# Optimization experiments

Hardware: AMD Instinct MI355X
Metric: run time of the kernel (lower is better)

Reference implementation:

```python
import jax, jax.numpy as jnp
import numpy as np

T, D_IN, NE = 131072, 1024, 64

def setup_inputs() -> dict:
    key = jax.random.key(0)
    k1, k2 = jax.random.split(key)
    x = jax.random.normal(k1, (T, D_IN), dtype=jnp.float32)
    W = jax.random.normal(k2, (NE, D_IN), dtype=jnp.float32) * (1.0 / np.sqrt(D_IN))
    return {"x": x, "W": W, "top_k": 2}

def reference(x, W, top_k):
    # fp32 router logits: [T, Ne]
    logits = jnp.einsum('td,ed->te', x.astype(jnp.float32), W.astype(jnp.float32))
    k = min(int(top_k), W.shape[0])
    vals, idx = jax.lax.top_k(logits, k)           # [T, k] each
    w = jax.nn.softmax(vals, axis=-1).astype(x.dtype)
    return (idx, w)
```

## Files before the change

### kernel.cpp

```cpp
#include <hip/hip_runtime.h>
#include <math.h>

constexpr int T_TOKENS = 131072;
constexpr int D        = 1024;
constexpr float EPS_GAP = 1e-3f;

typedef __attribute__((ext_vector_type(8))) short bf16x8;
typedef __attribute__((ext_vector_type(4))) float f32x4;
typedef __bf16 bf16v8 __attribute__((ext_vector_type(8)));
typedef float  f32v8  __attribute__((ext_vector_type(8)));

__device__ __forceinline__ void split2(const float4 lo, const float4 hi,
                                       bf16x8& p0, bf16x8& p1) {
    f32v8 f = {lo.x, lo.y, lo.z, lo.w, hi.x, hi.y, hi.z, hi.w};
    bf16v8 h0 = __builtin_convertvector(f, bf16v8);
    f32v8 back = __builtin_convertvector(h0, f32v8);
    bf16v8 h1 = __builtin_convertvector(f - back, bf16v8);
    p0 = __builtin_bit_cast(bf16x8, h0);
    p1 = __builtin_bit_cast(bf16x8, h1);
}

__global__ void prep_w(const float* __restrict__ W, bf16x8* __restrict__ wpl) {
    const int g = blockIdx.x;
    const int c = threadIdx.x >> 6;
    const int l = threadIdx.x & 63;
    const int e  = c * 16 + (l & 15);
    const int k0 = g * 32 + (l >> 4) * 8;
    const float4 lo = *(const float4*)(W + (long)e * D + k0);
    const float4 hi = *(const float4*)(W + (long)e * D + k0 + 4);
    bf16x8 p0, p1; split2(lo, hi, p0, p1);
    const int base = ((g * 4 + c) * 2) * 64 + l;
    wpl[base]      = p0;
    wpl[base + 64] = p1;
}

__global__ __launch_bounds__(256, 2)
void router_mfma(const float* __restrict__ x, const bf16x8* __restrict__ wpl,
                 float* __restrict__ out, unsigned* __restrict__ wcnt,
                 unsigned* __restrict__ wlist, unsigned cap)
{
    __shared__ __align__(16) char Xs[4][2][8192];

    const int tid = threadIdx.x;
    const int wv  = tid >> 6;
    const int l   = tid & 63;
    const int lg  = l >> 4;
    const int lr  = l & 15;
    const long t0 = (long)blockIdx.x * 128 + wv * 32;
    const int swz = (lr & 7) << 4;

    f32x4 acc[2][4];
#pragma unroll
    for (int a = 0; a < 2; ++a)
#pragma unroll
        for (int c = 0; c < 4; ++c) acc[a][c] = f32x4{0.f, 0.f, 0.f, 0.f};

    const int sil = (l & 15) * 16;
    const int sir = l >> 4;
    const char* xb = (const char*)x;

#define STAGE(S, BUF)                                                          \
    {                                                                          \
        _Pragma("unroll")                                                      \
        for (int i = 0; i < 8; ++i) {                                          \
            const int rr = 4 * i + sir;                                        \
            const char* src = xb + (t0 + rr) * 4096L + (S) * 256               \
                              + (sil ^ ((rr & 7) << 4));                       \
            char* dst = &Xs[wv][BUF][i * 1024];                                \
            __builtin_amdgcn_global_load_lds(                                  \
                (const __attribute__((address_space(1))) void*)src,            \
                (__attribute__((address_space(3))) void*)dst, 16, 0, 0);       \
        }                                                                      \
    }

#define SUBSTEP(SUB, W)                                                        \
    {                                                                          \
        const int c0 = (SUB) * 128 + lg * 32;                                  \
        const float4 lo0 = *(const float4*)(wb + lr * 256 + ((c0) ^ swz));     \
        const float4 hi0 = *(const float4*)(wb + lr * 256 + ((c0 + 16) ^ swz));\
        const float4 lo1 = *(const float4*)(wb + (16 + lr) * 256 + ((c0) ^ swz));     \
        const float4 hi1 = *(const float4*)(wb + (16 + lr) * 256 + ((c0 + 16) ^ swz));\
        bf16x8 a00, a01, a10, a11;                                             \
        split2(lo0, hi0, a00, a01);                                            \
        split2(lo1, hi1, a10, a11);                                            \
        _Pragma("unroll")                                                      \
        for (int c = 0; c < 4; ++c) {                                          \
            acc[0][c] = __builtin_amdgcn_mfma_f32_16x16x32_bf16(a00, W[c*2+0], acc[0][c], 0, 0, 0); \
            acc[0][c] = __builtin_amdgcn_mfma_f32_16x16x32_bf16(a01, W[c*2+0], acc[0][c], 0, 0, 0); \
            acc[0][c] = __builtin_amdgcn_mfma_f32_16x16x32_bf16(a00, W[c*2+1], acc[0][c], 0, 0, 0); \
            acc[1][c] = __builtin_amdgcn_mfma_f32_16x16x32_bf16(a10, W[c*2+0], acc[1][c], 0, 0, 0); \
            acc[1][c] = __builtin_amdgcn_mfma_f32_16x16x32_bf16(a11, W[c*2+0], acc[1][c], 0, 0, 0); \
            acc[1][c] = __builtin_amdgcn_mfma_f32_16x16x32_bf16(a10, W[c*2+1], acc[1][c], 0, 0, 0); \
        }                                                                      \
    }

    STAGE(0, 0);

#pragma unroll 1
    for (int s = 0; s < 16; ++s) {
        const int buf = s & 1;
        bf16x8 w0[8], w1[8];
#pragma unroll
        for (int c = 0; c < 4; ++c) {
            w0[c * 2 + 0] = wpl[(size_t)(2 * s) * 512 + (c * 2 + 0) * 64 + l];
            w0[c * 2 + 1] = wpl[(size_t)(2 * s) * 512 + (c * 2 + 1) * 64 + l];
            w1[c * 2 + 0] = wpl[(size_t)(2 * s + 1) * 512 + (c * 2 + 0) * 64 + l];
            w1[c * 2 + 1] = wpl[(size_t)(2 * s + 1) * 512 + (c * 2 + 1) * 64 + l];
        }
        const int sn = (s + 1 < 16) ? s + 1 : 15;
        if (buf) { STAGE(sn, 0) } else { STAGE(sn, 1) }
        asm volatile("s_waitcnt vmcnt(24)" ::: "memory");
        __builtin_amdgcn_sched_barrier(0);
        const char* wb = &Xs[wv][buf][0];
        SUBSTEP(0, w0)
        SUBSTEP(1, w1)
    }
#undef SUBSTEP
#undef STAGE

#pragma unroll
    for (int a = 0; a < 2; ++a)
#pragma unroll
    for (int r = 0; r < 4; ++r) {
        float v1 = acc[a][0][r]; int i1 = lr;
        float v2 = -INFINITY;    int i2 = 1 << 20;
        float v3 = -INFINITY;
#pragma unroll
        for (int c = 1; c < 4; ++c) {
            const float v = acc[a][c][r]; const int e = lr + 16 * c;
            if (v > v1)      { v3 = v2; v2 = v1; i2 = i1; v1 = v; i1 = e; }
            else if (v > v2) { v3 = v2; v2 = v;  i2 = e; }
            else if (v > v3) { v3 = v; }
        }
#pragma unroll
        for (int m = 8; m >= 1; m >>= 1) {
            const float ov1 = __shfl_xor(v1, m);
            const int   oi1 = __shfl_xor(i1, m);
            const float ov2 = __shfl_xor(v2, m);
            const int   oi2 = __shfl_xor(i2, m);
            const float ov3 = __shfl_xor(v3, m);
            const bool tv = v1 >= ov1;
            const float x2 = tv ? v2 : ov2, x3 = tv ? v3 : ov3;
            const float y1 = tv ? ov1 : v1, y2 = tv ? ov2 : v2;
            const float nv3 = (x2 >= y1) ? fmaxf(x3, y1) : fmaxf(x2, y2);
            const bool aw = (ov1 > v1) || (ov1 == v1 && oi1 < i1);
            const float nv1 = aw ? ov1 : v1; const int ni1 = aw ? oi1 : i1;
            const float c1v = aw ? v1  : ov1; const int c1i = aw ? i1  : oi1;
            const float c2v = aw ? ov2 : v2;  const int c2i = aw ? oi2 : i2;
            const bool bw = (c1v > c2v) || (c1v == c2v && c1i < c2i);
            v1 = nv1; i1 = ni1;
            v2 = bw ? c1v : c2v; i2 = bw ? c1i : c2i;
            v3 = nv3;
        }
        if (lr == 0) {
            const long t = t0 + a * 16 + lg * 4 + r;
            const float e  = expf(v2 - v1);
            const float dn = 1.0f + e;
            out[t * 2 + 0] = (float)i1;
            out[t * 2 + 1] = (float)i2;
            out[(long)T_TOKENS * 2 + t * 2 + 0] = 1.0f / dn;
            out[(long)T_TOKENS * 2 + t * 2 + 1] = e / dn;
            if (v1 - v2 < EPS_GAP || v2 - v3 < EPS_GAP) {
                const unsigned p = atomicAdd(wcnt, 1u);
                if (p < cap) wlist[p] = (unsigned)t;
            }
        }
    }
}

__global__ __launch_bounds__(256)
void router_fixup(const float* __restrict__ x, const float* __restrict__ W,
                  float* __restrict__ out, const unsigned* __restrict__ wcnt,
                  const unsigned* __restrict__ wlist, unsigned cap)
{
    __shared__ float ps[4][64];
    unsigned cnt = wcnt[0]; if (cnt > cap) cnt = cap;
    const int wv = threadIdx.x >> 6;
    const int l  = threadIdx.x & 63;
    const int kb = (wv == 0) ? 0 : (wv == 1) ? 320 : (wv == 2) ? 640 : 832;
    const int ke = (wv == 0) ? 320 : (wv == 1) ? 640 : (wv == 2) ? 832 : 1024;

    for (unsigned it = blockIdx.x; it < cnt; it += gridDim.x) {
        const long t = (long)wlist[it];
        const float* xr = x + t * (long)D;
        const float* wr = W + (long)l * D;
        float accP = 0.f;
#pragma unroll 4
        for (int k = kb; k < ke; k += 4) {
            const float4 xv = *(const float4*)(xr + k);
            const float4 wvv = *(const float4*)(wr + k);
            accP = fmaf(xv.x, wvv.x, accP);
            accP = fmaf(xv.y, wvv.y, accP);
            accP = fmaf(xv.z, wvv.z, accP);
            accP = fmaf(xv.w, wvv.w, accP);
        }
        ps[wv][l] = accP;
        __syncthreads();
        if (wv == 0) {
            const float accT = __fadd_rn(__fadd_rn(__fadd_rn(ps[0][l], ps[1][l]), ps[2][l]), ps[3][l]);
            float v1 = accT; int i1 = l;
            float v2 = -INFINITY; int i2 = 1 << 20;
#pragma unroll
            for (int m = 32; m >= 1; m >>= 1) {
                const float ov1 = __shfl_xor(v1, m);
                const int   oi1 = __shfl_xor(i1, m);
                const float ov2 = __shfl_xor(v2, m);
                const int   oi2 = __shfl_xor(i2, m);
                const bool aw = (ov1 > v1) || (ov1 == v1 && oi1 < i1);
                const float nv1 = aw ? ov1 : v1; const int ni1 = aw ? oi1 : i1;
                const float c1v = aw ? v1  : ov1; const int c1i = aw ? i1  : oi1;
                const float c2v = aw ? ov2 : v2;  const int c2i = aw ? oi2 : i2;
                const bool bw = (c1v > c2v) || (c1v == c2v && c1i < c2i);
                v1 = nv1; i1 = ni1;
                v2 = bw ? c1v : c2v; i2 = bw ? c1i : c2i;
            }
            if (l == 0) {
                const float e  = expf(v2 - v1);
                const float dn = 1.0f + e;
                out[t * 2 + 0] = (float)i1;
                out[t * 2 + 1] = (float)i2;
                out[(long)T_TOKENS * 2 + t * 2 + 0] = 1.0f / dn;
                out[(long)T_TOKENS * 2 + t * 2 + 1] = e / dn;
            }
        }
        __syncthreads();
    }
}

extern "C" void kernel_launch(void* const* d_in, const int* in_sizes, int n_in,
                              void* d_out, int out_size, void* d_ws, size_t ws_size,
                              hipStream_t stream) {
    const float* x = (const float*)d_in[0];
    const float* W = (const float*)d_in[1];
    float* out = (float*)d_out;

    unsigned* wcnt  = (unsigned*)d_ws;
    bf16x8*   wpl   = (bf16x8*)((char*)d_ws + 1024);
    unsigned* wlist = (unsigned*)((char*)d_ws + 1024 + 262144);
    size_t rem = (ws_size - 1024 - 262144) / 4;
    unsigned cap = (unsigned)(rem > (1u << 22) ? (1u << 22) : rem);

    (void)hipMemsetAsync(d_ws, 0, 64, stream);
    prep_w<<<dim3(32), dim3(256), 0, stream>>>(W, wpl);
    router_mfma<<<dim3(T_TOKENS / 128), dim3(256), 0, stream>>>(x, wpl, out, wcnt, wlist, cap);
    router_fixup<<<dim3(512), dim3(256), 0, stream>>>(x, W, out, wcnt, wlist, cap);
}
```

Baseline: 191.4 us.

## Halve tokens per wave and double K-chunk per pipeline stage

Each wave now handles 16 tokens instead of 32, and each stage loads 128 floats of K per token instead of 64, giving 8 pipeline iterations with 4 substeps each. The grid doubles to T/64 blocks, so there is more parallelism and fewer, larger stages with less loop overhead. The cost is that the W fragments fetched per iteration are reused across only one 16-token tile instead of two, doubling W traffic per token, and 32 bf16x8 W registers are held at once, which adds register pressure.

Result: slower. 203.9 us (+6.5%).

```diff
diff --git a/kernel.cpp b/kernel.cpp
--- a/kernel.cpp
+++ b/kernel.cpp
@@ -46,25 +46,21 @@
     const int l   = tid & 63;
     const int lg  = l >> 4;
     const int lr  = l & 15;
-    const long t0 = (long)blockIdx.x * 128 + wv * 32;
+    const long t0 = (long)blockIdx.x * 64 + wv * 16;
     const int swz = (lr & 7) << 4;
-
-    f32x4 acc[2][4];
-#pragma unroll
-    for (int a = 0; a < 2; ++a)
-#pragma unroll
-        for (int c = 0; c < 4; ++c) acc[a][c] = f32x4{0.f, 0.f, 0.f, 0.f};
-
-    const int sil = (l & 15) * 16;
-    const int sir = l >> 4;
+    const int sil = (l & 31) * 16;
     const char* xb = (const char*)x;
+
+    f32x4 acc[4];
+#pragma unroll
+    for (int c = 0; c < 4; ++c) acc[c] = f32x4{0.f, 0.f, 0.f, 0.f};
 
 #define STAGE(S, BUF)                                                          \
     {                                                                          \
         _Pragma("unroll")                                                      \
         for (int i = 0; i < 8; ++i) {                                          \
-            const int rr = 4 * i + sir;                                        \
-            const char* src = xb + (t0 + rr) * 4096L + (S) * 256               \
+            const int rr = 2 * i + (l >> 5);                                   \
+            const char* src = xb + (t0 + rr) * 4096L + (S) * 512               \
                               + (sil ^ ((rr & 7) << 4));                       \
             char* dst = &Xs[wv][BUF][i * 1024];                                \
             __builtin_amdgcn_global_load_lds(                                  \
@@ -73,61 +69,52 @@
         }                                                                      \
     }
 
-#define SUBSTEP(SUB, W)                                                        \
+#define SUBSTEP(SUB)                                                           \
     {                                                                          \
         const int c0 = (SUB) * 128 + lg * 32;                                  \
-        const float4 lo0 = *(const float4*)(wb + lr * 256 + ((c0) ^ swz));     \
-        const float4 hi0 = *(const float4*)(wb + lr * 256 + ((c0 + 16) ^ swz));\
-        const float4 lo1 = *(const float4*)(wb + (16 + lr) * 256 + ((c0) ^ swz));     \
-        const float4 hi1 = *(const float4*)(wb + (16 + lr) * 256 + ((c0 + 16) ^ swz));\
-        bf16x8 a00, a01, a10, a11;                                             \
-        split2(lo0, hi0, a00, a01);                                            \
-        split2(lo1, hi1, a10, a11);                                            \
+        const float4 lo = *(const float4*)(wb + lr * 512 + (c0 ^ swz));        \
+        const float4 hi = *(const float4*)(wb + lr * 512 + ((c0 + 16) ^ swz)); \
+        bf16x8 a0, a1;                                                         \
+        split2(lo, hi, a0, a1);                                                \
         _Pragma("unroll")                                                      \
         for (int c = 0; c < 4; ++c) {                                          \
-            acc[0][c] = __builtin_amdgcn_mfma_f32_16x16x32_bf16(a00, W[c*2+0], acc[0][c], 0, 0, 0); \
-            acc[0][c] = __builtin_amdgcn_mfma_f32_16x16x32_bf16(a01, W[c*2+0], acc[0][c], 0, 0, 0); \
-            acc[0][c] = __builtin_amdgcn_mfma_f32_16x16x32_bf16(a00, W[c*2+1], acc[0][c], 0, 0, 0); \
-            acc[1][c] = __builtin_amdgcn_mfma_f32_16x16x32_bf16(a10, W[c*2+0], acc[1][c], 0, 0, 0); \
-            acc[1][c] = __builtin_amdgcn_mfma_f32_16x16x32_bf16(a11, W[c*2+0], acc[1][c], 0, 0, 0); \
-            acc[1][c] = __builtin_amdgcn_mfma_f32_16x16x32_bf16(a10, W[c*2+1], acc[1][c], 0, 0, 0); \
+            acc[c] = __builtin_amdgcn_mfma_f32_16x16x32_bf16(a0, w[SUB][c*2+0], acc[c], 0, 0, 0); \
+            acc[c] = __builtin_amdgcn_mfma_f32_16x16x32_bf16(a1, w[SUB][c*2+0], acc[c], 0, 0, 0); \
+            acc[c] = __builtin_amdgcn_mfma_f32_16x16x32_bf16(a0, w[SUB][c*2+1], acc[c], 0, 0, 0); \
         }                                                                      \
     }
 
     STAGE(0, 0);
 
 #pragma unroll 1
-    for (int s = 0; s < 16; ++s) {
+    for (int s = 0; s < 8; ++s) {
         const int buf = s & 1;
-        bf16x8 w0[8], w1[8];
-#pragma unroll
-        for (int c = 0; c < 4; ++c) {
-            w0[c * 2 + 0] = wpl[(size_t)(2 * s) * 512 + (c * 2 + 0) * 64 + l];
-            w0[c * 2 + 1] = wpl[(size_t)(2 * s) * 512 + (c * 2 + 1) * 64 + l];
-            w1[c * 2 + 0] = wpl[(size_t)(2 * s + 1) * 512 + (c * 2 + 0) * 64 + l];
-            w1[c * 2 + 1] = wpl[(size_t)(2 * s + 1) * 512 + (c * 2 + 1) * 64 + l];
-        }
-        const int sn = (s + 1 < 16) ? s + 1 : 15;
-        if (buf) { STAGE(sn, 0) } else { STAGE(sn, 1) }
+        bf16x8 w[4][8];
+#pragma unroll
+        for (int g = 0; g < 4; ++g)
+#pragma unroll
+            for (int q = 0; q < 8; ++q)
+                w[g][q] = wpl[(size_t)(s * 4 + g) * 512 + q * 64 + l];
+        if (s + 1 < 8) { if (buf) STAGE(s + 1, 0) else STAGE(s + 1, 1) }
         asm volatile("s_waitcnt vmcnt(24)" ::: "memory");
         __builtin_amdgcn_sched_barrier(0);
         const char* wb = &Xs[wv][buf][0];
-        SUBSTEP(0, w0)
-        SUBSTEP(1, w1)
+        SUBSTEP(0)
+        SUBSTEP(1)
+        SUBSTEP(2)
+        SUBSTEP(3)
     }
 #undef SUBSTEP
 #undef STAGE
 
 #pragma unroll
-    for (int a = 0; a < 2; ++a)
-#pragma unroll
     for (int r = 0; r < 4; ++r) {
-        float v1 = acc[a][0][r]; int i1 = lr;
-        float v2 = -INFINITY;    int i2 = 1 << 20;
+        float v1 = acc[0][r]; int i1 = lr;
+        float v2 = -INFINITY;  int i2 = 1 << 20;
         float v3 = -INFINITY;
 #pragma unroll
         for (int c = 1; c < 4; ++c) {
-            const float v = acc[a][c][r]; const int e = lr + 16 * c;
+            const float v = acc[c][r]; const int e = lr + 16 * c;
             if (v > v1)      { v3 = v2; v2 = v1; i2 = i1; v1 = v; i1 = e; }
             else if (v > v2) { v3 = v2; v2 = v;  i2 = e; }
             else if (v > v3) { v3 = v; }
@@ -153,7 +140,7 @@
             v3 = nv3;
         }
         if (lr == 0) {
-            const long t = t0 + a * 16 + lg * 4 + r;
+            const long t = t0 + lg * 4 + r;
             const float e  = expf(v2 - v1);
             const float dn = 1.0f + e;
             out[t * 2 + 0] = (float)i1;
@@ -242,6 +229,6 @@
 
     (void)hipMemsetAsync(d_ws, 0, 64, stream);
     prep_w<<<dim3(32), dim3(256), 0, stream>>>(W, wpl);
-    router_mfma<<<dim3(T_TOKENS / 128), dim3(256), 0, stream>>>(x, wpl, out, wcnt, wlist, cap);
+    router_mfma<<<dim3(T_TOKENS / 64), dim3(256), 0, stream>>>(x, wpl, out, wcnt, wlist, cap);
     router_fixup<<<dim3(512), dim3(256), 0, stream>>>(x, W, out, wcnt, wlist, cap);
 }
```

## Halve K-chunk per stage and double occupancy target to four blocks per SIMD

Applied to the files above, without the earlier changes.

Each pipeline stage now covers 32 floats of K per token instead of 64, which halves the per-wave LDS staging buffer and runs 32 stages instead of 16. The W-register preload per iteration drops from 16 to 8 vectors and the launch bound rises to four blocks per CU. The aim is more resident waves to hide global-load latency in this memory-bound pass. In exchange, each stage waits on fewer in-flight loads and there are twice as many iterations, so per-iteration loop and wait overhead grows.

Measured after the change: 196.4 us. 1.03x slower.

```diff
diff --git a/kernel.cpp b/kernel.cpp
--- a/kernel.cpp
+++ b/kernel.cpp
@@ -34,12 +34,12 @@
     wpl[base + 64] = p1;
 }
 
-__global__ __launch_bounds__(256, 2)
+__global__ __launch_bounds__(256, 4)
 void router_mfma(const float* __restrict__ x, const bf16x8* __restrict__ wpl,
                  float* __restrict__ out, unsigned* __restrict__ wcnt,
                  unsigned* __restrict__ wlist, unsigned cap)
 {
-    __shared__ __align__(16) char Xs[4][2][8192];
+    __shared__ __align__(16) char Xs[4][2][4096];
 
     const int tid = threadIdx.x;
     const int wv  = tid >> 6;
@@ -48,24 +48,21 @@
     const int lr  = l & 15;
     const long t0 = (long)blockIdx.x * 128 + wv * 32;
     const int swz = (lr & 7) << 4;
+    const char* xb = (const char*)x;
 
     f32x4 acc[2][4];
 #pragma unroll
     for (int a = 0; a < 2; ++a)
 #pragma unroll
         for (int c = 0; c < 4; ++c) acc[a][c] = f32x4{0.f, 0.f, 0.f, 0.f};
-
-    const int sil = (l & 15) * 16;
-    const int sir = l >> 4;
-    const char* xb = (const char*)x;
 
 #define STAGE(S, BUF)                                                          \
     {                                                                          \
         _Pragma("unroll")                                                      \
-        for (int i = 0; i < 8; ++i) {                                          \
-            const int rr = 4 * i + sir;                                        \
-            const char* src = xb + (t0 + rr) * 4096L + (S) * 256               \
-                              + (sil ^ ((rr & 7) << 4));                       \
+        for (int i = 0; i < 4; ++i) {                                          \
+            const int rr = 8 * i + (l >> 3);                                   \
+            const char* src = xb + (t0 + rr) * 4096L + (S) * 128               \
+                              + (((l & 7) * 16) ^ ((rr & 7) << 4));            \
             char* dst = &Xs[wv][BUF][i * 1024];                                \
             __builtin_amdgcn_global_load_lds(                                  \
                 (const __attribute__((address_space(1))) void*)src,            \
@@ -73,49 +70,36 @@
         }                                                                      \
     }
 
-#define SUBSTEP(SUB, W)                                                        \
-    {                                                                          \
-        const int c0 = (SUB) * 128 + lg * 32;                                  \
-        const float4 lo0 = *(const float4*)(wb + lr * 256 + ((c0) ^ swz));     \
-        const float4 hi0 = *(const float4*)(wb + lr * 256 + ((c0 + 16) ^ swz));\
-        const float4 lo1 = *(const float4*)(wb + (16 + lr) * 256 + ((c0) ^ swz));     \
-        const float4 hi1 = *(const float4*)(wb + (16 + lr) * 256 + ((c0 + 16) ^ swz));\
-        bf16x8 a00, a01, a10, a11;                                             \
-        split2(lo0, hi0, a00, a01);                                            \
-        split2(lo1, hi1, a10, a11);                                            \
-        _Pragma("unroll")                                                      \
-        for (int c = 0; c < 4; ++c) {                                          \
-            acc[0][c] = __builtin_amdgcn_mfma_f32_16x16x32_bf16(a00, W[c*2+0], acc[0][c], 0, 0, 0); \
-            acc[0][c] = __builtin_amdgcn_mfma_f32_16x16x32_bf16(a01, W[c*2+0], acc[0][c], 0, 0, 0); \
-            acc[0][c] = __builtin_amdgcn_mfma_f32_16x16x32_bf16(a00, W[c*2+1], acc[0][c], 0, 0, 0); \
-            acc[1][c] = __builtin_amdgcn_mfma_f32_16x16x32_bf16(a10, W[c*2+0], acc[1][c], 0, 0, 0); \
-            acc[1][c] = __builtin_amdgcn_mfma_f32_16x16x32_bf16(a11, W[c*2+0], acc[1][c], 0, 0, 0); \
-            acc[1][c] = __builtin_amdgcn_mfma_f32_16x16x32_bf16(a10, W[c*2+1], acc[1][c], 0, 0, 0); \
-        }                                                                      \
-    }
-
     STAGE(0, 0);
 
 #pragma unroll 1
-    for (int s = 0; s < 16; ++s) {
+    for (int s = 0; s < 32; ++s) {
         const int buf = s & 1;
-        bf16x8 w0[8], w1[8];
-#pragma unroll
-        for (int c = 0; c < 4; ++c) {
-            w0[c * 2 + 0] = wpl[(size_t)(2 * s) * 512 + (c * 2 + 0) * 64 + l];
-            w0[c * 2 + 1] = wpl[(size_t)(2 * s) * 512 + (c * 2 + 1) * 64 + l];
-            w1[c * 2 + 0] = wpl[(size_t)(2 * s + 1) * 512 + (c * 2 + 0) * 64 + l];
-            w1[c * 2 + 1] = wpl[(size_t)(2 * s + 1) * 512 + (c * 2 + 1) * 64 + l];
-        }
-        const int sn = (s + 1 < 16) ? s + 1 : 15;
+        bf16x8 w[8];
+#pragma unroll
+        for (int q = 0; q < 8; ++q)
+            w[q] = wpl[(size_t)s * 512 + q * 64 + l];
+        const int sn = (s + 1 < 32) ? s + 1 : 31;
         if (buf) { STAGE(sn, 0) } else { STAGE(sn, 1) }
-        asm volatile("s_waitcnt vmcnt(24)" ::: "memory");
+        asm volatile("s_waitcnt vmcnt(12)" ::: "memory");
         __builtin_amdgcn_sched_barrier(0);
-        const char* wb = &Xs[wv][buf][0];
-        SUBSTEP(0, w0)
-        SUBSTEP(1, w1)
-    }
-#undef SUBSTEP
+        const char* ab = &Xs[wv][buf][0];
+#pragma unroll
+        for (int a = 0; a < 2; ++a) {
+            const char* rowp = ab + (a * 16 + lr) * 128;
+            const int c0 = lg * 32;
+            const float4 lo = *(const float4*)(rowp + (c0 ^ swz));
+            const float4 hi = *(const float4*)(rowp + ((c0 + 16) ^ swz));
+            bf16x8 a0, a1;
+            split2(lo, hi, a0, a1);
+#pragma unroll
+            for (int c = 0; c < 4; ++c) {
+                acc[a][c] = __builtin_amdgcn_mfma_f32_16x16x32_bf16(a0, w[c*2+0], acc[a][c], 0, 0, 0);
+                acc[a][c] = __builtin_amdgcn_mfma_f32_16x16x32_bf16(a1, w[c*2+0], acc[a][c], 0, 0, 0);
+                acc[a][c] = __builtin_amdgcn_mfma_f32_16x16x32_bf16(a0, w[c*2+1], acc[a][c], 0, 0, 0);
+            }
+        }
+    }
 #undef STAGE
 
 #pragma unroll
```
